# Kernel tuning notes

Hardware: AMD Instinct MI355X
Metric: run time of the kernel (lower is better)

## Reference

```python
import jax, jax.numpy as jnp
import numpy as np

B = 512
MIRROR_C1_OFFSET = -1.2432432432432432

def make_ff(batch):
    ff = jnp.zeros((1, 1, 60, 60), jnp.float32)
    ff = ff.at[0, 0, :, 41:51].set(0.5)
    ff = ff.at[0, 0, :, 51:].set(1.0)
    return jnp.broadcast_to(ff, (batch, 1, 60, 60))

def conv_valid(x, w, b):
    y = jax.lax.conv_general_dilated(x, w, (1, 1), 'VALID',
                                     dimension_numbers=('NCHW', 'OIHW', 'NCHW'))
    return y + b[None, :, None, None]

def build_padded(x, h, ff):
    # (B,3,92,92) canvas with custom mirror padding (channel-dependent sign on left)
    b = x.shape[0]
    inner = jnp.concatenate([x, h, ff], axis=1)  # (B,3,60,60)
    h2 = jnp.zeros((b, 3, 92, 92), x.dtype)
    h2 = h2.at[:, :, 16:76, 16:76].set(inner)
    h2 = h2.at[:, :, 16:76, 76:].set(h2[:, :, 16:76, 60:76][..., ::-1])
    h2 = h2.at[:, :, 76:, 16:].set(h2[:, :, 60:76, 16:][:, :, ::-1, :])
    h2 = h2.at[:, :, :16, 16:].set(0.0)
    left = h2[:, :, :, 16:32][..., ::-1]  # mirror across col 16
    h2 = h2.at[:, 0, :, :16].set(left[:, 0])
    h2 = h2.at[:, 2, :, :16].set(left[:, 2])
    h2 = h2.at[:, 1, :, :16].set(MIRROR_C1_OFFSET - left[:, 1])
    return h2

def powerlayer(x, h, ff, w1, b1, w2, b2, w3, b3, w4, b4):
    h2 = build_padded(x, h, ff)
    h2 = jax.nn.relu(conv_valid(h2, w1, b1))  # (B,8,84,84)
    h2 = jax.nn.relu(conv_valid(h2, w2, b2))  # (B,8,76,76)
    h2 = jax.nn.relu(conv_valid(h2, w3, b3))  # (B,8,68,68)
    h2 = conv_valid(h2, w4, b4)               # (B,1,60,60)
    return h2

def setup_inputs() -> dict:
    key = jax.random.key(0)
    ks = jax.random.split(key, 10)
    x = jax.random.normal(ks[0], (B, 1, 60, 60), jnp.float32)
    fc_w = jax.random.normal(ks[1], (3600, 3600), jnp.float32) * (1.0 / 60.0)
    fc_b = jax.random.normal(ks[2], (3600,), jnp.float32) * 0.01
    w1 = jax.random.normal(ks[3], (8, 3, 9, 9), jnp.float32) * (1.0 / np.sqrt(3 * 81))
    bC1 = jnp.zeros((8,), jnp.float32)
    w2 = jax.random.normal(ks[4], (8, 8, 9, 9), jnp.float32) * (1.0 / np.sqrt(8 * 81))
    bC2 = jnp.zeros((8,), jnp.float32)
    w3 = jax.random.normal(ks[5], (8, 8, 9, 9), jnp.float32) * (1.0 / np.sqrt(8 * 81))
    bC3 = jnp.zeros((8,), jnp.float32)
    w4 = jax.random.normal(ks[6], (1, 8, 9, 9), jnp.float32) * (1.0 / np.sqrt(8 * 81))
    bC4 = jnp.zeros((1,), jnp.float32)
    return {"x": x, "fc_w": fc_w, "fc_b": fc_b,
            "w1": w1, "bC1": bC1, "w2": w2, "bC2": bC2,
            "w3": w3, "bC3": bC3, "w4": w4, "bC4": bC4}

def reference(x, fc_w, fc_b, w1, bC1, w2, bC2, w3, bC3, w4, bC4):
    b = x.shape[0]
    ff = make_ff(b)
    h = jax.nn.relu(x.reshape(b, 3600) @ fc_w.T + fc_b)
    h = h.reshape(b, 1, 60, 60)
    for _ in range(5):
        h = powerlayer(x, h, ff, w1, bC1, w2, bC2, w3, bC3, w4, bC4)
    return h.reshape(b, 60, 60)
```

## Files before the change

### kernel.cpp

```cpp
#include <hip/hip_runtime.h>

#define B_IMG 512
#define C1OFF (-1.2432432432432432f)

__device__ __forceinline__ float relu_(float v) { return v > 0.f ? v : 0.f; }

__device__ __forceinline__ void loadrow12(const float* __restrict__ p, float r[12]) {
    float4 a = *(const float4*)(p);
    float4 b = *(const float4*)(p + 4);
    float4 c = *(const float4*)(p + 8);
    r[0]=a.x; r[1]=a.y; r[2]=a.z;  r[3]=a.w;
    r[4]=b.x; r[5]=b.y; r[6]=b.z;  r[7]=b.w;
    r[8]=c.x; r[9]=c.y; r[10]=c.z; r[11]=c.w;
}

__global__ __launch_bounds__(256) void fc_kernel(
    const float* __restrict__ X, const float* __restrict__ W,
    const float* __restrict__ Bv, float* __restrict__ H)
{
    __shared__ __align__(16) float As[16][68];
    __shared__ __align__(16) float Bs[16][68];
    const int tid = threadIdx.x;
    const int m0 = blockIdx.y * 64;
    const int n0 = blockIdx.x * 64;
    const int tm = tid >> 4, tn = tid & 15;
    const int lr = tid >> 2;
    const int lk = (tid & 3) << 2;
    const bool bvalid = (n0 + lr) < 3600;
    const float* Arow = X + (size_t)(m0 + lr) * 3600 + lk;
    const float* Brow = W + (size_t)(bvalid ? (n0 + lr) : 0) * 3600 + lk;
    float acc[4][4] = {};
    for (int k0 = 0; k0 < 3600; k0 += 16) {
        float4 av = *(const float4*)(Arow + k0);
        float4 bv = make_float4(0.f, 0.f, 0.f, 0.f);
        if (bvalid) bv = *(const float4*)(Brow + k0);
        __syncthreads();
        As[lk + 0][lr] = av.x; As[lk + 1][lr] = av.y;
        As[lk + 2][lr] = av.z; As[lk + 3][lr] = av.w;
        Bs[lk + 0][lr] = bv.x; Bs[lk + 1][lr] = bv.y;
        Bs[lk + 2][lr] = bv.z; Bs[lk + 3][lr] = bv.w;
        __syncthreads();
        #pragma unroll
        for (int kk = 0; kk < 16; ++kk) {
            float a[4], b[4];
            *(float4*)a = *(const float4*)&As[kk][tm << 2];
            *(float4*)b = *(const float4*)&Bs[kk][tn << 2];
            #pragma unroll
            for (int i = 0; i < 4; ++i)
                #pragma unroll
                for (int j = 0; j < 4; ++j)
                    acc[i][j] = fmaf(a[i], b[j], acc[i][j]);
        }
    }
    #pragma unroll
    for (int i = 0; i < 4; ++i) {
        int m = m0 + (tm << 2) + i;
        #pragma unroll
        for (int j = 0; j < 4; ++j) {
            int n = n0 + (tn << 2) + j;
            if (n < 3600) {
                float v = acc[i][j] + Bv[n];
                H[(size_t)m * 3600 + n] = relu_(v);
            }
        }
    }
}

__device__ __forceinline__ float pad_core(const float* __restrict__ xb,
                                          const float* __restrict__ hb,
                                          int ch, int r, int c)
{
    if (r < 16) return 0.f;
    int rr = (r <= 75) ? r : (151 - r);
    int cc = (c <= 75) ? c : (151 - c);
    int i = rr - 16, j = cc - 16;
    if (ch == 0) return xb[i * 60 + j];
    if (ch == 1) return hb[i * 60 + j];
    return (j >= 51) ? 1.0f : ((j >= 41) ? 0.5f : 0.0f);
}

__device__ __forceinline__ float pad_val(const float* __restrict__ xb,
                                         const float* __restrict__ hb,
                                         int ch, int r, int c)
{
    if (c >= 16) return pad_core(xb, hb, ch, r, c);
    float v = pad_core(xb, hb, ch, r, 31 - c);
    return (ch == 1) ? (C1OFF - v) : v;
}

__global__ __launch_bounds__(256) void pad_kernel(
    const float* __restrict__ x, const float* __restrict__ h,
    float* __restrict__ pad)
{
    const int b = blockIdx.x;
    const float* xb = x + (size_t)b * 3600;
    const float* hb = h + (size_t)b * 3600;
    float* pb = pad + (size_t)b * (3 * 92 * 92);
    for (int i = threadIdx.x; i < 3 * 92 * 92; i += 256) {
        int ch = i / 8464;
        int rem = i - ch * 8464;
        int r = rem / 92;
        int c = rem - r * 92;
        pb[i] = pad_val(xb, hb, ch, r, c);
    }
}

template<int IC, int IH, bool RELU>
__global__ __launch_bounds__(256, 4) void convA(
    const float* __restrict__ in, const float* __restrict__ wt,
    const float* __restrict__ bias, float* __restrict__ out)
{
    constexpr int IW = IH, OH = IH - 8, OW = OH;
    constexpr int NGX = OW / 4, NP = OH * NGX;
    const int b = blockIdx.y;
    int p = blockIdx.x * 256 + threadIdx.x;
    const bool act = (p < NP);
    if (!act) p = NP - 1;
    const int oy = p / NGX;
    const int x0 = (p - oy * NGX) * 4;
    const float* ib = in + (size_t)b * IC * IH * IW + (size_t)oy * IW + x0;

    float acc[8][4];
    #pragma unroll
    for (int oc = 0; oc < 8; ++oc) {
        float bv = bias[oc];
        #pragma unroll
        for (int j = 0; j < 4; ++j) acc[oc][j] = bv;
    }

    #pragma unroll 1
    for (int ic = 0; ic < IC; ++ic) {
        const float* rp = ib + (size_t)ic * IH * IW;
        const float* wb = wt + ic * 81;
        #pragma unroll
        for (int ky = 0; ky < 9; ++ky) {
            float r[12];
            loadrow12(rp + ky * IW, r);
            #pragma unroll
            for (int oc = 0; oc < 8; ++oc) {
                #pragma unroll
                for (int kx = 0; kx < 9; ++kx) {
                    float w = wb[oc * (IC * 81) + ky * 9 + kx];
                    #pragma unroll
                    for (int j = 0; j < 4; ++j)
                        acc[oc][j] = fmaf(w, r[kx + j], acc[oc][j]);
                }
            }
        }
    }

    if (act) {
        #pragma unroll
        for (int oc = 0; oc < 8; ++oc) {
            float* ob = out + ((size_t)b * 8 + oc) * (OH * OW)
                        + (size_t)oy * OW + x0;
            float4 v;
            if (RELU) {
                v = make_float4(relu_(acc[oc][0]), relu_(acc[oc][1]),
                                relu_(acc[oc][2]), relu_(acc[oc][3]));
            } else {
                v = make_float4(acc[oc][0], acc[oc][1], acc[oc][2], acc[oc][3]);
            }
            *(float4*)&ob[0] = v;
        }
    }
}

#define BSTEP(TOP, BOT, KY)                                        \
    do {                                                           \
        loadrow12(rp + ((KY) + 1) * IW, (BOT));                    \
        _Pragma("unroll")                                          \
        for (int kx = 0; kx < 9; ++kx) {                           \
            float w = wb[(KY) * 9 + kx];                           \
            _Pragma("unroll")                                      \
            for (int j = 0; j < 4; ++j) {                          \
                acc0[j] = fmaf(w, (TOP)[kx + j], acc0[j]);         \
                acc1[j] = fmaf(w, (BOT)[kx + j], acc1[j]);         \
            }                                                      \
        }                                                          \
    } while (0)

__global__ __launch_bounds__(256, 4) void convB(
    const float* __restrict__ in, const float* __restrict__ wt,
    const float* __restrict__ bias, float* __restrict__ out)
{
    constexpr int IH = 68, IW = 68, OW = 60;
    constexpr int NGX = 15, NP = 450;
    const int b = blockIdx.y;
    int p = blockIdx.x * 256 + threadIdx.x;
    const bool act = (p < NP);
    if (!act) p = NP - 1;
    const int gy = p / NGX;
    const int gx = p - gy * NGX;
    const int oy = gy * 2, x0 = gx * 4;
    const float* ib = in + (size_t)b * 8 * IH * IW + (size_t)oy * IW + x0;

    float bv = bias[0];
    float acc0[4] = {bv, bv, bv, bv}, acc1[4] = {bv, bv, bv, bv};

    #pragma unroll 1
    for (int ic = 0; ic < 8; ++ic) {
        const float* rp = ib + (size_t)ic * IH * IW;
        const float* wb = wt + ic * 81;
        float rA[12], rB[12];
        loadrow12(rp, rA);
        BSTEP(rA, rB, 0); BSTEP(rB, rA, 1); BSTEP(rA, rB, 2);
        BSTEP(rB, rA, 3); BSTEP(rA, rB, 4); BSTEP(rB, rA, 5);
        BSTEP(rA, rB, 6); BSTEP(rB, rA, 7); BSTEP(rA, rB, 8);
    }

    if (act) {
        float* ob = out + (size_t)b * 3600 + (size_t)oy * OW + x0;
        *(float4*)&ob[0]  = make_float4(acc0[0], acc0[1], acc0[2], acc0[3]);
        *(float4*)&ob[OW] = make_float4(acc1[0], acc1[1], acc1[2], acc1[3]);
    }
}

extern "C" void kernel_launch(void* const* d_in, const int* in_sizes, int n_in,
                              void* d_out, int out_size, void* d_ws, size_t ws_size,
                              hipStream_t stream)
{
    const float* x   = (const float*)d_in[0];
    const float* fcw = (const float*)d_in[1];
    const float* fcb = (const float*)d_in[2];
    const float* w1  = (const float*)d_in[3];
    const float* b1  = (const float*)d_in[4];
    const float* w2  = (const float*)d_in[5];
    const float* b2  = (const float*)d_in[6];
    const float* w3  = (const float*)d_in[7];
    const float* b3  = (const float*)d_in[8];
    const float* w4  = (const float*)d_in[9];
    const float* b4  = (const float*)d_in[10];

    float* h = (float*)d_out;

    const size_t PADN = 3 * 92 * 92;
    const size_t T1N  = 8 * 84 * 84;
    const size_t T2N  = 8 * 76 * 76;
    size_t per_img = (PADN + T1N + T2N) * sizeof(float);
    int CH = (int)(ws_size / per_img);
    if (CH > B_IMG) CH = B_IMG;
    if (CH < 1) CH = 1;
    float* pad = (float*)d_ws;
    float* t1  = pad + (size_t)CH * PADN;
    float* t2  = t1 + (size_t)CH * T1N;

    fc_kernel<<<dim3(57, 8), 256, 0, stream>>>(x, fcw, fcb, h);

    for (int it = 0; it < 5; ++it) {
        for (int c0 = 0; c0 < B_IMG; c0 += CH) {
            int cn = (B_IMG - c0) < CH ? (B_IMG - c0) : CH;
            pad_kernel<<<cn, 256, 0, stream>>>(x + (size_t)c0 * 3600,
                                               h + (size_t)c0 * 3600, pad);
            convA<3, 92, true><<<dim3(7, cn), 256, 0, stream>>>(pad, w1, b1, t1);
            convA<8, 84, true><<<dim3(6, cn), 256, 0, stream>>>(t1, w2, b2, t2);
            convA<8, 76, true><<<dim3(5, cn), 256, 0, stream>>>(t2, w3, b3, t1);
            convB<<<dim3(2, cn), 256, 0, stream>>>(t1, w4, b4,
                                                   h + (size_t)c0 * 3600);
        }
    }
}
```

Before: 4.125 ms.

## Compute two output rows per thread in conv layers with flattened image-tile grid

The 8-output-channel conv kernel now computes a 2x4 output tile per thread and reuses each loaded input row for two adjacent output rows through a rolling two-buffer scheme. This roughly halves global/L1 row loads and weight reads per output. Thread indexing is flattened across images, so the grid no longer wastes partial blocks per image. The cost is a doubled accumulator array (64 floats), which raises register pressure, so the occupancy hint drops from 4 to 3 blocks per SM.

```diff
diff --git a/kernel.cpp b/kernel.cpp
--- a/kernel.cpp
+++ b/kernel.cpp
@@ -105,48 +105,60 @@
     }
 }
 
+#define A2STEP(TOP, BOT, KY)                                               \
+    do {                                                                   \
+        loadrow12(rp + ((KY) + 1) * IW, (BOT));                            \
+        _Pragma("unroll")                                                  \
+        for (int oc = 0; oc < 8; ++oc) {                                   \
+            _Pragma("unroll")                                              \
+            for (int kx = 0; kx < 9; ++kx) {                               \
+                float w = wb[oc * (IC * 81) + (KY) * 9 + kx];              \
+                _Pragma("unroll")                                          \
+                for (int j = 0; j < 4; ++j) {                              \
+                    acc[oc][0][j] = fmaf(w, (TOP)[kx + j], acc[oc][0][j]); \
+                    acc[oc][1][j] = fmaf(w, (BOT)[kx + j], acc[oc][1][j]); \
+                }                                                          \
+            }                                                              \
+        }                                                                  \
+    } while (0)
+
 template<int IC, int IH, bool RELU>
-__global__ __launch_bounds__(256, 4) void convA(
+__global__ __launch_bounds__(256, 3) void convA2(
     const float* __restrict__ in, const float* __restrict__ wt,
-    const float* __restrict__ bias, float* __restrict__ out)
+    const float* __restrict__ bias, float* __restrict__ out, int nimg)
 {
     constexpr int IW = IH, OH = IH - 8, OW = OH;
-    constexpr int NGX = OW / 4, NP = OH * NGX;
-    const int b = blockIdx.y;
-    int p = blockIdx.x * 256 + threadIdx.x;
-    const bool act = (p < NP);
-    if (!act) p = NP - 1;
-    const int oy = p / NGX;
-    const int x0 = (p - oy * NGX) * 4;
+    constexpr int NGX = OW / 4, NGY = OH / 2, NPB = NGX * NGY;
+    const int p0 = blockIdx.x * 256 + threadIdx.x;
+    const int total = nimg * NPB;
+    const bool act = (p0 < total);
+    const int p = act ? p0 : (total - 1);
+    const int b = p / NPB;
+    const int rem = p - b * NPB;
+    const int gy = rem / NGX;
+    const int gx = rem - gy * NGX;
+    const int oy = gy * 2, x0 = gx * 4;
     const float* ib = in + (size_t)b * IC * IH * IW + (size_t)oy * IW + x0;
 
-    float acc[8][4];
+    float acc[8][2][4];
     #pragma unroll
     for (int oc = 0; oc < 8; ++oc) {
         float bv = bias[oc];
         #pragma unroll
-        for (int j = 0; j < 4; ++j) acc[oc][j] = bv;
+        for (int r = 0; r < 2; ++r)
+            #pragma unroll
+            for (int j = 0; j < 4; ++j) acc[oc][r][j] = bv;
     }
 
     #pragma unroll 1
     for (int ic = 0; ic < IC; ++ic) {
         const float* rp = ib + (size_t)ic * IH * IW;
         const float* wb = wt + ic * 81;
-        #pragma unroll
-        for (int ky = 0; ky < 9; ++ky) {
-            float r[12];
-            loadrow12(rp + ky * IW, r);
-            #pragma unroll
-            for (int oc = 0; oc < 8; ++oc) {
-                #pragma unroll
-                for (int kx = 0; kx < 9; ++kx) {
-                    float w = wb[oc * (IC * 81) + ky * 9 + kx];
-                    #pragma unroll
-                    for (int j = 0; j < 4; ++j)
-                        acc[oc][j] = fmaf(w, r[kx + j], acc[oc][j]);
-                }
-            }
-        }
+        float rA[12], rB[12];
+        loadrow12(rp, rA);
+        A2STEP(rA, rB, 0); A2STEP(rB, rA, 1); A2STEP(rA, rB, 2);
+        A2STEP(rB, rA, 3); A2STEP(rA, rB, 4); A2STEP(rB, rA, 5);
+        A2STEP(rA, rB, 6); A2STEP(rB, rA, 7); A2STEP(rA, rB, 8);
     }
 
     if (act) {
@@ -154,14 +166,18 @@
         for (int oc = 0; oc < 8; ++oc) {
             float* ob = out + ((size_t)b * 8 + oc) * (OH * OW)
                         + (size_t)oy * OW + x0;
-            float4 v;
-            if (RELU) {
-                v = make_float4(relu_(acc[oc][0]), relu_(acc[oc][1]),
-                                relu_(acc[oc][2]), relu_(acc[oc][3]));
-            } else {
-                v = make_float4(acc[oc][0], acc[oc][1], acc[oc][2], acc[oc][3]);
+            #pragma unroll
+            for (int r = 0; r < 2; ++r) {
+                float4 v;
+                if (RELU) {
+                    v = make_float4(relu_(acc[oc][r][0]), relu_(acc[oc][r][1]),
+                                    relu_(acc[oc][r][2]), relu_(acc[oc][r][3]));
+                } else {
+                    v = make_float4(acc[oc][r][0], acc[oc][r][1],
+                                    acc[oc][r][2], acc[oc][r][3]);
+                }
+                *(float4*)&ob[(size_t)r * OW] = v;
             }
-            *(float4*)&ob[0] = v;
         }
     }
 }
@@ -252,9 +268,12 @@
             int cn = (B_IMG - c0) < CH ? (B_IMG - c0) : CH;
             pad_kernel<<<cn, 256, 0, stream>>>(x + (size_t)c0 * 3600,
                                                h + (size_t)c0 * 3600, pad);
-            convA<3, 92, true><<<dim3(7, cn), 256, 0, stream>>>(pad, w1, b1, t1);
-            convA<8, 84, true><<<dim3(6, cn), 256, 0, stream>>>(t1, w2, b2, t2);
-            convA<8, 76, true><<<dim3(5, cn), 256, 0, stream>>>(t2, w3, b3, t1);
+            int g1 = (cn * 882 + 255) / 256;
+            int g2 = (cn * 722 + 255) / 256;
+            int g3 = (cn * 578 + 255) / 256;
+            convA2<3, 92, true><<<g1, 256, 0, stream>>>(pad, w1, b1, t1, cn);
+            convA2<8, 84, true><<<g2, 256, 0, stream>>>(t1, w2, b2, t2, cn);
+            convA2<8, 76, true><<<g3, 256, 0, stream>>>(t2, w3, b3, t1, cn);
             convB<<<dim3(2, cn), 256, 0, stream>>>(t1, w4, b4,
                                                    h + (size_t)c0 * 3600);
         }
```

Result: slower. 4.765 ms (+15.5%).

## Use packed FP32 FMA with even/odd weight split and flat grid for convolutions

Applied to the files above, without the earlier changes.

Rewrites the convolution kernels to use 2-wide packed float FMA (v_pk_fma_f32). Weights are pre-split into even/odd taps and duplicated into float2 pairs, and shifted row vectors are loaded unaligned so that output pairs line up with input pairs. It also flattens the grid across images to cut tail waste and replaces the specialised last-layer kernel with the generic one. In exchange it adds weight-prep launches and unaligned loads, and lowers the occupancy hint from 4 to 3.

```diff
diff --git a/kernel.cpp b/kernel.cpp
--- a/kernel.cpp
+++ b/kernel.cpp
@@ -3,16 +3,13 @@
 #define B_IMG 512
 #define C1OFF (-1.2432432432432432f)
 
+typedef __attribute__((ext_vector_type(2))) float f2;
+typedef __attribute__((ext_vector_type(2), aligned(4))) float f2u;
+typedef __attribute__((ext_vector_type(4))) float f4;
+typedef __attribute__((ext_vector_type(4), aligned(4))) float f4u;
+
 __device__ __forceinline__ float relu_(float v) { return v > 0.f ? v : 0.f; }
-
-__device__ __forceinline__ void loadrow12(const float* __restrict__ p, float r[12]) {
-    float4 a = *(const float4*)(p);
-    float4 b = *(const float4*)(p + 4);
-    float4 c = *(const float4*)(p + 8);
-    r[0]=a.x; r[1]=a.y; r[2]=a.z;  r[3]=a.w;
-    r[4]=b.x; r[5]=b.y; r[6]=b.z;  r[7]=b.w;
-    r[8]=c.x; r[9]=c.y; r[10]=c.z; r[11]=c.w;
-}
+__device__ __forceinline__ f2 mk2(float a, float b) { f2 r; r[0] = a; r[1] = b; return r; }
 
 __global__ __launch_bounds__(256) void fc_kernel(
     const float* __restrict__ X, const float* __restrict__ W,
@@ -66,6 +63,20 @@
     }
 }
 
+__global__ __launch_bounds__(256) void prep_pk(
+    const float* __restrict__ w, int OC, int IC, f2* __restrict__ out)
+{
+    int n = IC * 9 * OC * 9;
+    for (int t = threadIdx.x + blockIdx.x * 256; t < n; t += gridDim.x * 256) {
+        int q = t % 9; int rest = t / 9;
+        int oc = rest % OC; rest /= OC;
+        int ky = rest % 9; int ic = rest / 9;
+        const float* ws = w + (((size_t)oc * IC + ic) * 9 + ky) * 9;
+        float v = (q < 5) ? ws[2 * q] : ws[2 * (q - 5) + 1];
+        out[t] = mk2(v, v);
+    }
+}
+
 __device__ __forceinline__ float pad_core(const float* __restrict__ xb,
                                           const float* __restrict__ hb,
                                           int ch, int r, int c)
@@ -105,45 +116,65 @@
     }
 }
 
-template<int IC, int IH, bool RELU>
-__global__ __launch_bounds__(256, 4) void convA(
-    const float* __restrict__ in, const float* __restrict__ wt,
-    const float* __restrict__ bias, float* __restrict__ out)
+template<int IC, int OC, int IH, bool RELU>
+__global__ __launch_bounds__(256, 3) void convP(
+    const float* __restrict__ in, const f2* __restrict__ wpk,
+    const float* __restrict__ bias, float* __restrict__ out, int total)
 {
     constexpr int IW = IH, OH = IH - 8, OW = OH;
-    constexpr int NGX = OW / 4, NP = OH * NGX;
-    const int b = blockIdx.y;
-    int p = blockIdx.x * 256 + threadIdx.x;
-    const bool act = (p < NP);
-    if (!act) p = NP - 1;
-    const int oy = p / NGX;
-    const int x0 = (p - oy * NGX) * 4;
+    constexpr int NGX = OW / 4, NPB = OH * NGX;
+    const int p0 = blockIdx.x * 256 + threadIdx.x;
+    const bool act = (p0 < total);
+    const int p = act ? p0 : (total - 1);
+    const int b = p / NPB;
+    const int rem = p - b * NPB;
+    const int oy = rem / NGX;
+    const int x0 = (rem - oy * NGX) * 4;
     const float* ib = in + (size_t)b * IC * IH * IW + (size_t)oy * IW + x0;
 
-    float acc[8][4];
+    f2 acc[OC][2];
     #pragma unroll
-    for (int oc = 0; oc < 8; ++oc) {
+    for (int oc = 0; oc < OC; ++oc) {
         float bv = bias[oc];
-        #pragma unroll
-        for (int j = 0; j < 4; ++j) acc[oc][j] = bv;
+        acc[oc][0] = mk2(bv, bv);
+        acc[oc][1] = mk2(bv, bv);
     }
 
     #pragma unroll 1
     for (int ic = 0; ic < IC; ++ic) {
         const float* rp = ib + (size_t)ic * IH * IW;
-        const float* wb = wt + ic * 81;
+        const f2* wq0 = wpk + (size_t)ic * 9 * OC * 9;
         #pragma unroll
         for (int ky = 0; ky < 9; ++ky) {
-            float r[12];
-            loadrow12(rp + ky * IW, r);
+            const float* row = rp + ky * IW;
+            f4 e0 = *(const f4*)(row);
+            f4 e1 = *(const f4*)(row + 4);
+            f4 e2 = *(const f4*)(row + 8);
+            f4u s0 = *(const f4u*)(row + 1);
+            f4u s1 = *(const f4u*)(row + 5);
+            f2u s2 = *(const f2u*)(row + 9);
+            f2 re[6], sh[5];
+            re[0] = mk2(e0[0], e0[1]); re[1] = mk2(e0[2], e0[3]);
+            re[2] = mk2(e1[0], e1[1]); re[3] = mk2(e1[2], e1[3]);
+            re[4] = mk2(e2[0], e2[1]); re[5] = mk2(e2[2], e2[3]);
+            sh[0] = mk2(s0[0], s0[1]); sh[1] = mk2(s0[2], s0[3]);
+            sh[2] = mk2(s1[0], s1[1]); sh[3] = mk2(s1[2], s1[3]);
+            sh[4] = mk2(s2[0], s2[1]);
+            const f2* wq = wq0 + ky * OC * 9;
             #pragma unroll
-            for (int oc = 0; oc < 8; ++oc) {
+            for (int oc = 0; oc < OC; ++oc) {
+                const f2* w9 = wq + oc * 9;
                 #pragma unroll
-                for (int kx = 0; kx < 9; ++kx) {
-                    float w = wb[oc * (IC * 81) + ky * 9 + kx];
-                    #pragma unroll
-                    for (int j = 0; j < 4; ++j)
-                        acc[oc][j] = fmaf(w, r[kx + j], acc[oc][j]);
+                for (int m = 0; m < 5; ++m) {
+                    f2 w = w9[m];
+                    acc[oc][0] = __builtin_elementwise_fma(w, re[m], acc[oc][0]);
+                    acc[oc][1] = __builtin_elementwise_fma(w, re[m + 1], acc[oc][1]);
+                }
+                #pragma unroll
+                for (int m = 0; m < 4; ++m) {
+                    f2 w = w9[5 + m];
+                    acc[oc][0] = __builtin_elementwise_fma(w, sh[m], acc[oc][0]);
+                    acc[oc][1] = __builtin_elementwise_fma(w, sh[m + 1], acc[oc][1]);
                 }
             }
         }
@@ -151,68 +182,14 @@
 
     if (act) {
         #pragma unroll
-        for (int oc = 0; oc < 8; ++oc) {
-            float* ob = out + ((size_t)b * 8 + oc) * (OH * OW)
+        for (int oc = 0; oc < OC; ++oc) {
+            float* ob = out + ((size_t)b * OC + oc) * (OH * OW)
                         + (size_t)oy * OW + x0;
-            float4 v;
-            if (RELU) {
-                v = make_float4(relu_(acc[oc][0]), relu_(acc[oc][1]),
-                                relu_(acc[oc][2]), relu_(acc[oc][3]));
-            } else {
-                v = make_float4(acc[oc][0], acc[oc][1], acc[oc][2], acc[oc][3]);
-            }
-            *(float4*)&ob[0] = v;
-        }
-    }
-}
-
-#define BSTEP(TOP, BOT, KY)                                        \
-    do {                                                           \
-        loadrow12(rp + ((KY) + 1) * IW, (BOT));                    \
-        _Pragma("unroll")                                          \
-        for (int kx = 0; kx < 9; ++kx) {                           \
-            float w = wb[(KY) * 9 + kx];                           \
-            _Pragma("unroll")                                      \
-            for (int j = 0; j < 4; ++j) {                          \
-                acc0[j] = fmaf(w, (TOP)[kx + j], acc0[j]);         \
-                acc1[j] = fmaf(w, (BOT)[kx + j], acc1[j]);         \
-            }                                                      \
-        }                                                          \
-    } while (0)
-
-__global__ __launch_bounds__(256, 4) void convB(
-    const float* __restrict__ in, const float* __restrict__ wt,
-    const float* __restrict__ bias, float* __restrict__ out)
-{
-    constexpr int IH = 68, IW = 68, OW = 60;
-    constexpr int NGX = 15, NP = 450;
-    const int b = blockIdx.y;
-    int p = blockIdx.x * 256 + threadIdx.x;
-    const bool act = (p < NP);
-    if (!act) p = NP - 1;
-    const int gy = p / NGX;
-    const int gx = p - gy * NGX;
-    const int oy = gy * 2, x0 = gx * 4;
-    const float* ib = in + (size_t)b * 8 * IH * IW + (size_t)oy * IW + x0;
-
-    float bv = bias[0];
-    float acc0[4] = {bv, bv, bv, bv}, acc1[4] = {bv, bv, bv, bv};
-
-    #pragma unroll 1
-    for (int ic = 0; ic < 8; ++ic) {
-        const float* rp = ib + (size_t)ic * IH * IW;
-        const float* wb = wt + ic * 81;
-        float rA[12], rB[12];
-        loadrow12(rp, rA);
-        BSTEP(rA, rB, 0); BSTEP(rB, rA, 1); BSTEP(rA, rB, 2);
-        BSTEP(rB, rA, 3); BSTEP(rA, rB, 4); BSTEP(rB, rA, 5);
-        BSTEP(rA, rB, 6); BSTEP(rB, rA, 7); BSTEP(rA, rB, 8);
-    }
-
-    if (act) {
-        float* ob = out + (size_t)b * 3600 + (size_t)oy * OW + x0;
-        *(float4*)&ob[0]  = make_float4(acc0[0], acc0[1], acc0[2], acc0[3]);
-        *(float4*)&ob[OW] = make_float4(acc1[0], acc1[1], acc1[2], acc1[3]);
+            float v0 = acc[oc][0][0], v1 = acc[oc][0][1];
+            float v2 = acc[oc][1][0], v3 = acc[oc][1][1];
+            if (RELU) { v0 = relu_(v0); v1 = relu_(v1); v2 = relu_(v2); v3 = relu_(v3); }
+            *(float4*)ob = make_float4(v0, v1, v2, v3);
+        }
     }
 }
 
@@ -234,16 +211,28 @@
 
     float* h = (float*)d_out;
 
+    f2* wp1 = (f2*)d_ws;
+    f2* wp2 = wp1 + 4096;
+    f2* wp3 = wp2 + 8192;
+    f2* wp4 = wp3 + 8192;
+    float* fbase = (float*)((char*)d_ws + 262144);
+    size_t avail = (ws_size - 262144) / sizeof(float);
+
     const size_t PADN = 3 * 92 * 92;
     const size_t T1N  = 8 * 84 * 84;
     const size_t T2N  = 8 * 76 * 76;
-    size_t per_img = (PADN + T1N + T2N) * sizeof(float);
-    int CH = (int)(ws_size / per_img);
+    size_t per_img = PADN + T1N + T2N;
+    int CH = (int)(avail / per_img);
     if (CH > B_IMG) CH = B_IMG;
     if (CH < 1) CH = 1;
-    float* pad = (float*)d_ws;
+    float* pad = fbase;
     float* t1  = pad + (size_t)CH * PADN;
     float* t2  = t1 + (size_t)CH * T1N;
+
+    prep_pk<<<8, 256, 0, stream>>>(w1, 8, 3, wp1);
+    prep_pk<<<21, 256, 0, stream>>>(w2, 8, 8, wp2);
+    prep_pk<<<21, 256, 0, stream>>>(w3, 8, 8, wp3);
+    prep_pk<<<3, 256, 0, stream>>>(w4, 1, 8, wp4);
 
     fc_kernel<<<dim3(57, 8), 256, 0, stream>>>(x, fcw, fcb, h);
 
@@ -252,11 +241,15 @@
             int cn = (B_IMG - c0) < CH ? (B_IMG - c0) : CH;
             pad_kernel<<<cn, 256, 0, stream>>>(x + (size_t)c0 * 3600,
                                                h + (size_t)c0 * 3600, pad);
-            convA<3, 92, true><<<dim3(7, cn), 256, 0, stream>>>(pad, w1, b1, t1);
-            convA<8, 84, true><<<dim3(6, cn), 256, 0, stream>>>(t1, w2, b2, t2);
-            convA<8, 76, true><<<dim3(5, cn), 256, 0, stream>>>(t2, w3, b3, t1);
-            convB<<<dim3(2, cn), 256, 0, stream>>>(t1, w4, b4,
-                                                   h + (size_t)c0 * 3600);
-        }
-    }
-}
+            int t1n = cn * 1764, t2n = cn * 1444, t3n = cn * 1156, t4n = cn * 900;
+            convP<3, 8, 92, true><<<(t1n + 255) / 256, 256, 0, stream>>>(
+                pad, wp1, b1, t1, t1n);
+            convP<8, 8, 84, true><<<(t2n + 255) / 256, 256, 0, stream>>>(
+                t1, wp2, b2, t2, t2n);
+            convP<8, 8, 76, true><<<(t3n + 255) / 256, 256, 0, stream>>>(
+                t2, wp3, b3, t1, t3n);
+            convP<8, 1, 68, false><<<(t4n + 255) / 256, 256, 0, stream>>>(
+                t1, wp4, b4, h + (size_t)c0 * 3600, t4n);
+        }
+    }
+}
```

Result: slower. 4.237 ms (+2.7%).
